# Performance work log

Measured on AMD Instinct MI355X. Metric: run time of the kernel, lower is better.

The kernel has to match this reference:

```python
import jax, jax.numpy as jnp
import numpy as np

COMM_DIM = 8
HIDDEN = 64
N = 2048


def setup_inputs() -> dict:
    key = jax.random.key(0)
    k_msg, k_w1, k_b1, k_w2, k_b2 = jax.random.split(key, 5)
    s1 = 1.0 / np.sqrt(2 * COMM_DIM)  # torch Linear default-ish scale
    s2 = 1.0 / np.sqrt(HIDDEN)
    return {
        "messages": jax.random.normal(k_msg, (N, COMM_DIM), dtype=jnp.float32),
        "W1": jax.random.normal(k_w1, (HIDDEN, 2 * COMM_DIM), dtype=jnp.float32) * s1,
        "b1": jax.random.normal(k_b1, (HIDDEN,), dtype=jnp.float32) * s1,
        "W2": jax.random.normal(k_w2, (COMM_DIM, HIDDEN), dtype=jnp.float32) * s2,
        "b2": jax.random.normal(k_b2, (COMM_DIM,), dtype=jnp.float32) * s2,
    }


def reference(messages, W1, b1, W2, b2):
    # edge_mlp(concat([m_i, m_j])) for all ordered pairs, mean over j != i.
    # Linear1 on the concat splits: concat([mi,mj]) @ W1^T = mi @ W1[:,:D]^T + mj @ W1[:,D:]^T
    n = messages.shape[0]
    X1 = jnp.einsum('nd,hd->nh', messages, W1[:, :COMM_DIM])   # [N, H] contribution of m_i
    X2 = jnp.einsum('nd,hd->nh', messages, W1[:, COMM_DIM:])   # [N, H] contribution of m_j
    # pairwise hidden: [N, N, H] (the dominant, memory-bound intermediate)
    H = jax.nn.relu(X1[:, None, :] + X2[None, :, :] + b1)
    S = H.sum(axis=1)                                          # [N, H] sum over all j (incl. j==i)
    D = jax.nn.relu(X1 + X2 + b1)                              # [N, H] the j==i diagonal term
    # agg_i = sum_{j!=i} (relu(...) @ W2^T + b2); then divide by (N-1)
    agg = jnp.einsum('nh,dh->nd', S - D, W2) + (n - 1) * b2
    return agg / (n - 1)
```

## Files before the change

kernel.cpp:

```cpp
#include <hip/hip_runtime.h>


#define NN 2048
#define HH 64
#define DD 8

#define ITILES 32
#define JCHUNKS 32
#define JCHUNK (NN / JCHUNKS)
#define INV_SCALE (0.5f / (float)(NN - 1))

__global__ void prep_kernel(const float* __restrict__ msg,
                            const float* __restrict__ W1,
                            const float* __restrict__ b1,
                            float* __restrict__ A,
                            float* __restrict__ X2,
                            float* __restrict__ out) {
    int idx = blockIdx.x * blockDim.x + threadIdx.x;
    if (idx < NN * DD) out[idx] = 0.f;
    int i = idx >> 6;
    int h = idx & 63;
    const float4* m4 = (const float4*)(msg + i * DD);
    const float4* w4 = (const float4*)(W1 + h * (2 * DD));
    float4 m0 = m4[0], m1 = m4[1];
    float4 w0 = w4[0], w1 = w4[1], w2 = w4[2], w3 = w4[3];
    float x1 = m0.x * w0.x + m0.y * w0.y + m0.z * w0.z + m0.w * w0.w
             + m1.x * w1.x + m1.y * w1.y + m1.z * w1.z + m1.w * w1.w;
    float x2 = m0.x * w2.x + m0.y * w2.y + m0.z * w2.z + m0.w * w2.w
             + m1.x * w3.x + m1.y * w3.y + m1.z * w3.z + m1.w * w3.w;
    A[idx]  = x1 + b1[h];
    X2[idx] = x2;
}

__global__ void __launch_bounds__(256, 4)
pair_fused(const float* __restrict__ A,
           const float* __restrict__ X2,
           const float* __restrict__ W2,
           const float* __restrict__ b2,
           float* __restrict__ out) {
    __shared__ float4 sX2[JCHUNK * 16];
    __shared__ float  T[64][68];
    __shared__ float4 sSXv[16];

    int it = blockIdx.x & (ITILES - 1);
    int jc = blockIdx.x >> 5;
    int hq = threadIdx.x & 15;
    int il = threadIdx.x >> 4;
    int h0 = hq * 4;
    int i0 = it * 64 + il * 4;
    bool des = (jc == it);

    {
        const float4* X2v = (const float4*)X2 + jc * JCHUNK * 16;
#pragma unroll
        for (int r = 0; r < 4; ++r) {
            int t = threadIdx.x + r * 256;
            sX2[t] = X2v[t];
        }
    }

    float a[4][4];
#pragma unroll
    for (int k = 0; k < 4; ++k) {
        float4 av = *(const float4*)&A[(i0 + k) * HH + h0];
        a[k][0] = av.x; a[k][1] = av.y; a[k][2] = av.z; a[k][3] = av.w;
    }
    float acc[4][4];
#pragma unroll
    for (int k = 0; k < 4; ++k)
#pragma unroll
        for (int hh = 0; hh < 4; ++hh)
            acc[k][hh] = 0.f;

    __syncthreads();

#pragma unroll 4
    for (int j = 0; j < JCHUNK; ++j) {
        float4 x = sX2[j * 16 + hq];
#pragma unroll
        for (int k = 0; k < 4; ++k) {
            acc[k][0] += __builtin_fabsf(a[k][0] + x.x);
            acc[k][1] += __builtin_fabsf(a[k][1] + x.y);
            acc[k][2] += __builtin_fabsf(a[k][2] + x.z);
            acc[k][3] += __builtin_fabsf(a[k][3] + x.w);
        }
    }

    const float* sX2f = (const float*)sX2;

    if (threadIdx.x < 64) {
        float s0 = 0.f, s1 = 0.f, s2 = 0.f, s3 = 0.f;
#pragma unroll 8
        for (int j = 0; j < JCHUNK; j += 4) {
            s0 += sX2f[(j + 0) * 64 + threadIdx.x];
            s1 += sX2f[(j + 1) * 64 + threadIdx.x];
            s2 += sX2f[(j + 2) * 64 + threadIdx.x];
            s3 += sX2f[(j + 3) * 64 + threadIdx.x];
        }
        ((float*)sSXv)[threadIdx.x] = (s0 + s1) + (s2 + s3);
    }

#pragma unroll
    for (int k = 0; k < 4; ++k) {
        float t0 = acc[k][0], t1 = acc[k][1], t2 = acc[k][2], t3 = acc[k][3];
        if (des) {
            int jl = il * 4 + k;
            float z0 = a[k][0] + sX2f[jl * 64 + h0 + 0];
            float z1 = a[k][1] + sX2f[jl * 64 + h0 + 1];
            float z2 = a[k][2] + sX2f[jl * 64 + h0 + 2];
            float z3 = a[k][3] + sX2f[jl * 64 + h0 + 3];
            t0 += (float)NN * a[k][0] - 2.f * (z0 > 0.f ? z0 : 0.f);
            t1 += (float)NN * a[k][1] - 2.f * (z1 > 0.f ? z1 : 0.f);
            t2 += (float)NN * a[k][2] - 2.f * (z2 > 0.f ? z2 : 0.f);
            t3 += (float)NN * a[k][3] - 2.f * (z3 > 0.f ? z3 : 0.f);
        }
        *(float4*)&T[il * 4 + k][h0] = make_float4(t0, t1, t2, t3);
    }
    __syncthreads();

    {
        int iL = threadIdx.x >> 3;
        int d  = threadIdx.x & 7;
        const float4* w2v = (const float4*)W2;
        float s0 = 0.f, s1 = 0.f, c = 0.f;
#pragma unroll
        for (int hb = 0; hb < 16; ++hb) {
            float4 w  = w2v[d * 16 + hb];
            float4 t0 = *(const float4*)&T[iL][hb * 4];
            float4 t1 = *(const float4*)&T[iL + 32][hb * 4];
            float4 sx = sSXv[hb];
            s0 += t0.x * w.x + t0.y * w.y + t0.z * w.z + t0.w * w.w;
            s1 += t1.x * w.x + t1.y * w.y + t1.z * w.z + t1.w * w.w;
            c  += sx.x * w.x + sx.y * w.y + sx.z * w.z + sx.w * w.w;
        }
        float v0 = (s0 + c) * INV_SCALE;
        float v1 = (s1 + c) * INV_SCALE;
        if (des) {
            float bv = b2[d];
            v0 += bv;
            v1 += bv;
        }
        int ibase = it * 64;
        atomicAdd(&out[(ibase + iL) * DD + d], v0);
        atomicAdd(&out[(ibase + iL + 32) * DD + d], v1);
    }
}

extern "C" void kernel_launch(void* const* d_in, const int* in_sizes, int n_in,
                              void* d_out, int out_size, void* d_ws, size_t ws_size,
                              hipStream_t stream) {
    const float* msg = (const float*)d_in[0];
    const float* W1  = (const float*)d_in[1];
    const float* b1  = (const float*)d_in[2];
    const float* W2  = (const float*)d_in[3];
    const float* b2  = (const float*)d_in[4];
    float* out = (float*)d_out;

    float* ws = (float*)d_ws;
    float* A  = ws;
    float* X2 = ws + NN * HH;

    prep_kernel<<<(NN * HH) / 256, 256, 0, stream>>>(msg, W1, b1, A, X2, out);
    pair_fused<<<ITILES * JCHUNKS, 256, 0, stream>>>(A, X2, W2, b2, out);
}
```

Measured before the change: 82.73 us.

## Fuse first-layer projection into pair kernel and drop prep kernel

```diff
diff --git a/kernel.cpp b/kernel.cpp
--- a/kernel.cpp
+++ b/kernel.cpp
@@ -10,31 +10,14 @@
 #define JCHUNK (NN / JCHUNKS)
 #define INV_SCALE (0.5f / (float)(NN - 1))
 
-__global__ void prep_kernel(const float* __restrict__ msg,
-                            const float* __restrict__ W1,
-                            const float* __restrict__ b1,
-                            float* __restrict__ A,
-                            float* __restrict__ X2,
-                            float* __restrict__ out) {
-    int idx = blockIdx.x * blockDim.x + threadIdx.x;
-    if (idx < NN * DD) out[idx] = 0.f;
-    int i = idx >> 6;
-    int h = idx & 63;
-    const float4* m4 = (const float4*)(msg + i * DD);
-    const float4* w4 = (const float4*)(W1 + h * (2 * DD));
-    float4 m0 = m4[0], m1 = m4[1];
-    float4 w0 = w4[0], w1 = w4[1], w2 = w4[2], w3 = w4[3];
-    float x1 = m0.x * w0.x + m0.y * w0.y + m0.z * w0.z + m0.w * w0.w
-             + m1.x * w1.x + m1.y * w1.y + m1.z * w1.z + m1.w * w1.w;
-    float x2 = m0.x * w2.x + m0.y * w2.y + m0.z * w2.z + m0.w * w2.w
-             + m1.x * w3.x + m1.y * w3.y + m1.z * w3.z + m1.w * w3.w;
-    A[idx]  = x1 + b1[h];
-    X2[idx] = x2;
+__device__ __forceinline__ float dot4(float4 a, float4 b) {
+    return a.x * b.x + a.y * b.y + a.z * b.z + a.w * b.w;
 }
 
 __global__ void __launch_bounds__(256, 4)
-pair_fused(const float* __restrict__ A,
-           const float* __restrict__ X2,
+pair_fused(const float* __restrict__ msg,
+           const float* __restrict__ W1,
+           const float* __restrict__ b1,
            const float* __restrict__ W2,
            const float* __restrict__ b2,
            float* __restrict__ out) {
@@ -50,21 +33,42 @@
     int i0 = it * 64 + il * 4;
     bool des = (jc == it);
 
-    {
-        const float4* X2v = (const float4*)X2 + jc * JCHUNK * 16;
+    const float4* m4 = (const float4*)msg;
+    const float4* w4 = (const float4*)W1;
+    float4 b1v = *(const float4*)&b1[h0];
+    float bb[4] = {b1v.x, b1v.y, b1v.z, b1v.w};
+
+    float4 wA[4][2], wB[4][2];
 #pragma unroll
-        for (int r = 0; r < 4; ++r) {
-            int t = threadIdx.x + r * 256;
-            sX2[t] = X2v[t];
-        }
+    for (int hh = 0; hh < 4; ++hh) {
+        wA[hh][0] = w4[(h0 + hh) * 4 + 0];
+        wA[hh][1] = w4[(h0 + hh) * 4 + 1];
+        wB[hh][0] = w4[(h0 + hh) * 4 + 2];
+        wB[hh][1] = w4[(h0 + hh) * 4 + 3];
     }
 
     float a[4][4];
 #pragma unroll
     for (int k = 0; k < 4; ++k) {
-        float4 av = *(const float4*)&A[(i0 + k) * HH + h0];
-        a[k][0] = av.x; a[k][1] = av.y; a[k][2] = av.z; a[k][3] = av.w;
+        float4 mi0 = m4[(i0 + k) * 2], mi1 = m4[(i0 + k) * 2 + 1];
+#pragma unroll
+        for (int hh = 0; hh < 4; ++hh)
+            a[k][hh] = dot4(mi0, wA[hh][0]) + dot4(mi1, wA[hh][1]) + bb[hh];
     }
+    {
+        int jg = jc * JCHUNK + il * 4;
+#pragma unroll
+        for (int k = 0; k < 4; ++k) {
+            float4 mj0 = m4[(jg + k) * 2], mj1 = m4[(jg + k) * 2 + 1];
+            float4 xv;
+            xv.x = dot4(mj0, wB[0][0]) + dot4(mj1, wB[0][1]);
+            xv.y = dot4(mj0, wB[1][0]) + dot4(mj1, wB[1][1]);
+            xv.z = dot4(mj0, wB[2][0]) + dot4(mj1, wB[2][1]);
+            xv.w = dot4(mj0, wB[3][0]) + dot4(mj1, wB[3][1]);
+            sX2[(il * 4 + k) * 16 + hq] = xv;
+        }
+    }
+
     float acc[4][4];
 #pragma unroll
     for (int k = 0; k < 4; ++k)
@@ -156,10 +160,6 @@
     const float* b2  = (const float*)d_in[4];
     float* out = (float*)d_out;
 
-    float* ws = (float*)d_ws;
-    float* A  = ws;
-    float* X2 = ws + NN * HH;
-
-    prep_kernel<<<(NN * HH) / 256, 256, 0, stream>>>(msg, W1, b1, A, X2, out);
-    pair_fused<<<ITILES * JCHUNKS, 256, 0, stream>>>(A, X2, W2, b2, out);
+    hipMemsetAsync(out, 0, NN * DD * sizeof(float), stream);
+    pair_fused<<<ITILES * JCHUNKS, 256, 0, stream>>>(msg, W1, b1, W2, b2, out);
 }
```

Measured after the change: 86.74 us. +4.8%, slower.

## Halve j-chunk size, replace LDS transpose epilogue with shuffle reduction

Applied to the files above, without the earlier changes.

```diff
diff --git a/kernel.cpp b/kernel.cpp
--- a/kernel.cpp
+++ b/kernel.cpp
@@ -6,7 +6,7 @@
 #define DD 8
 
 #define ITILES 32
-#define JCHUNKS 32
+#define JCHUNKS 64
 #define JCHUNK (NN / JCHUNKS)
 #define INV_SCALE (0.5f / (float)(NN - 1))
 
@@ -32,15 +32,14 @@
     X2[idx] = x2;
 }
 
-__global__ void __launch_bounds__(256, 4)
+__global__ void __launch_bounds__(256, 6)
 pair_fused(const float* __restrict__ A,
            const float* __restrict__ X2,
            const float* __restrict__ W2,
            const float* __restrict__ b2,
            float* __restrict__ out) {
-    __shared__ float4 sX2[JCHUNK * 16];
-    __shared__ float  T[64][68];
-    __shared__ float4 sSXv[16];
+    __shared__ float sX2f[JCHUNK * HH];
+    __shared__ float sSX[HH];
 
     int it = blockIdx.x & (ITILES - 1);
     int jc = blockIdx.x >> 5;
@@ -48,15 +47,12 @@
     int il = threadIdx.x >> 4;
     int h0 = hq * 4;
     int i0 = it * 64 + il * 4;
-    bool des = (jc == it);
 
     {
-        const float4* X2v = (const float4*)X2 + jc * JCHUNK * 16;
-#pragma unroll
-        for (int r = 0; r < 4; ++r) {
-            int t = threadIdx.x + r * 256;
-            sX2[t] = X2v[t];
-        }
+        const float4* src = (const float4*)(X2 + jc * JCHUNK * HH);
+        float4* dst = (float4*)sX2f;
+        dst[threadIdx.x]       = src[threadIdx.x];
+        dst[threadIdx.x + 256] = src[threadIdx.x + 256];
     }
 
     float a[4][4];
@@ -74,9 +70,10 @@
 
     __syncthreads();
 
+    const float4* sX2v = (const float4*)sX2f;
 #pragma unroll 4
     for (int j = 0; j < JCHUNK; ++j) {
-        float4 x = sX2[j * 16 + hq];
+        float4 x = sX2v[j * 16 + hq];
 #pragma unroll
         for (int k = 0; k < 4; ++k) {
             acc[k][0] += __builtin_fabsf(a[k][0] + x.x);
@@ -86,63 +83,71 @@
         }
     }
 
-    const float* sX2f = (const float*)sX2;
-
     if (threadIdx.x < 64) {
         float s0 = 0.f, s1 = 0.f, s2 = 0.f, s3 = 0.f;
-#pragma unroll 8
+#pragma unroll 4
         for (int j = 0; j < JCHUNK; j += 4) {
-            s0 += sX2f[(j + 0) * 64 + threadIdx.x];
-            s1 += sX2f[(j + 1) * 64 + threadIdx.x];
-            s2 += sX2f[(j + 2) * 64 + threadIdx.x];
-            s3 += sX2f[(j + 3) * 64 + threadIdx.x];
+            s0 += sX2f[(j + 0) * HH + threadIdx.x];
+            s1 += sX2f[(j + 1) * HH + threadIdx.x];
+            s2 += sX2f[(j + 2) * HH + threadIdx.x];
+            s3 += sX2f[(j + 3) * HH + threadIdx.x];
         }
-        ((float*)sSXv)[threadIdx.x] = (s0 + s1) + (s2 + s3);
+        sSX[threadIdx.x] = (s0 + s1) + (s2 + s3);
+    }
+    __syncthreads();
+
+    bool des = (jc == 2 * it + (il >> 3));
+    if (des) {
+        int jlb = (il & 7) * 4;
+#pragma unroll
+        for (int k = 0; k < 4; ++k) {
+            float4 xd = *(const float4*)&sX2f[(jlb + k) * HH + h0];
+            float z0 = a[k][0] + xd.x, z1 = a[k][1] + xd.y;
+            float z2 = a[k][2] + xd.z, z3 = a[k][3] + xd.w;
+            acc[k][0] += (float)NN * a[k][0] - 2.f * (z0 > 0.f ? z0 : 0.f);
+            acc[k][1] += (float)NN * a[k][1] - 2.f * (z1 > 0.f ? z1 : 0.f);
+            acc[k][2] += (float)NN * a[k][2] - 2.f * (z2 > 0.f ? z2 : 0.f);
+            acc[k][3] += (float)NN * a[k][3] - 2.f * (z3 > 0.f ? z3 : 0.f);
+        }
+    }
+
+    {
+        float4 sx = *(const float4*)&sSX[h0];
+#pragma unroll
+        for (int k = 0; k < 4; ++k) {
+            acc[k][0] += sx.x; acc[k][1] += sx.y;
+            acc[k][2] += sx.z; acc[k][3] += sx.w;
+        }
+    }
+
+    float4 w[8];
+    {
+        const float4* w2v = (const float4*)W2;
+#pragma unroll
+        for (int d = 0; d < 8; ++d)
+            w[d] = w2v[d * 16 + hq];
     }
 
 #pragma unroll
     for (int k = 0; k < 4; ++k) {
-        float t0 = acc[k][0], t1 = acc[k][1], t2 = acc[k][2], t3 = acc[k][3];
-        if (des) {
-            int jl = il * 4 + k;
-            float z0 = a[k][0] + sX2f[jl * 64 + h0 + 0];
-            float z1 = a[k][1] + sX2f[jl * 64 + h0 + 1];
-            float z2 = a[k][2] + sX2f[jl * 64 + h0 + 2];
-            float z3 = a[k][3] + sX2f[jl * 64 + h0 + 3];
-            t0 += (float)NN * a[k][0] - 2.f * (z0 > 0.f ? z0 : 0.f);
-            t1 += (float)NN * a[k][1] - 2.f * (z1 > 0.f ? z1 : 0.f);
-            t2 += (float)NN * a[k][2] - 2.f * (z2 > 0.f ? z2 : 0.f);
-            t3 += (float)NN * a[k][3] - 2.f * (z3 > 0.f ? z3 : 0.f);
+        float p[8];
+#pragma unroll
+        for (int d = 0; d < 8; ++d)
+            p[d] = acc[k][0] * w[d].x + acc[k][1] * w[d].y
+                 + acc[k][2] * w[d].z + acc[k][3] * w[d].w;
+#pragma unroll
+        for (int m = 1; m < 16; m <<= 1)
+#pragma unroll
+            for (int d = 0; d < 8; ++d)
+                p[d] += __shfl_xor(p[d], m);
+        if (hq == 0) {
+#pragma unroll
+            for (int d = 0; d < 8; ++d) {
+                float v = p[d] * INV_SCALE;
+                if (des) v += b2[d];
+                atomicAdd(&out[(i0 + k) * DD + d], v);
+            }
         }
-        *(float4*)&T[il * 4 + k][h0] = make_float4(t0, t1, t2, t3);
-    }
-    __syncthreads();
-
-    {
-        int iL = threadIdx.x >> 3;
-        int d  = threadIdx.x & 7;
-        const float4* w2v = (const float4*)W2;
-        float s0 = 0.f, s1 = 0.f, c = 0.f;
-#pragma unroll
-        for (int hb = 0; hb < 16; ++hb) {
-            float4 w  = w2v[d * 16 + hb];
-            float4 t0 = *(const float4*)&T[iL][hb * 4];
-            float4 t1 = *(const float4*)&T[iL + 32][hb * 4];
-            float4 sx = sSXv[hb];
-            s0 += t0.x * w.x + t0.y * w.y + t0.z * w.z + t0.w * w.w;
-            s1 += t1.x * w.x + t1.y * w.y + t1.z * w.z + t1.w * w.w;
-            c  += sx.x * w.x + sx.y * w.y + sx.z * w.z + sx.w * w.w;
-        }
-        float v0 = (s0 + c) * INV_SCALE;
-        float v1 = (s1 + c) * INV_SCALE;
-        if (des) {
-            float bv = b2[d];
-            v0 += bv;
-            v1 += bv;
-        }
-        int ibase = it * 64;
-        atomicAdd(&out[(ibase + iL) * DD + d], v0);
-        atomicAdd(&out[(ibase + iL + 32) * DD + d], v1);
     }
 }
 
```

Result: slower. 117.4 us (+41.9%).
